# Performance work log

Measured on AMD Instinct MI355X. Metric: run time of the kernel, lower is better.

## Reference

```python
import jax, jax.numpy as jnp
import numpy as np

B, TK, H = 32, 1024, 512
N = 2 * H          # hidden_dim * 2
AD = 512           # attention_dimension


def setup_inputs() -> dict:
    key = jax.random.key(0)
    ks = jax.random.split(key, 11)
    s = 0.02  # weight scale
    return {
        's_t_hat': jax.random.normal(ks[0], (B, N), jnp.float32),
        'encoder_outputs': jax.random.normal(ks[1], (B, TK, N), jnp.float32),
        'encoder_feature': jax.random.normal(ks[2], (B * TK, N), jnp.float32),
        'enc_padding_mask': jax.random.uniform(ks[3], (B, TK), jnp.float32),
        'coverage': jax.random.uniform(ks[4], (B, TK), jnp.float32),
        'r_i': jax.random.normal(ks[5], (B, TK, AD), jnp.float32),
        'W_s_w': jax.random.normal(ks[6], (N, N), jnp.float32) * s,
        'W_s_b': jax.random.normal(ks[7], (N,), jnp.float32) * s,
        'W_c_w': jax.random.normal(ks[8], (N, 1), jnp.float32) * s,
        'v_w': jax.random.normal(ks[9], (1, N), jnp.float32) * s,
        'W_r_w': jax.random.normal(ks[10], (N, AD), jnp.float32) * s,
    }


def reference(s_t_hat, encoder_outputs, encoder_feature, enc_padding_mask,
              coverage, r_i, W_s_w, W_s_b, W_c_w, v_w, W_r_w):
    b, t_k, n = encoder_outputs.shape
    # decoder feature: W_s(s_t_hat), broadcast over time
    dec_fea = s_t_hat @ W_s_w.T + W_s_b                       # [b, n]
    enc_feat = encoder_feature.reshape(b, t_k, n)             # [b, t_k, n]
    # coverage feature: W_c applied to scalar coverage per position
    cov_feat = coverage[..., None] * W_c_w[:, 0]              # [b, t_k, n]
    e = jnp.tanh(enc_feat + dec_fea[:, None, :] + cov_feat)   # [b, t_k, n]
    scores = jnp.einsum('btn,n->bt', e, v_w[0])               # [b, t_k]
    attn_ = jax.nn.softmax(scores, axis=1) * enc_padding_mask
    attn = attn_ / attn_.sum(1, keepdims=True)                # renormalized
    c_t = jnp.einsum('bt,btn->bn', attn, encoder_outputs)     # [b, n]
    coverage_new = coverage + attn                            # [b, t_k]
    # structural (LSA) branch
    Wrri = jnp.einsum('bta,na->btn', r_i, W_r_w)              # [b, t_k, n]
    e_s = jnp.tanh(Wrri + dec_fea[:, None, :])
    s2 = jnp.einsum('btn,n->bt', e_s, v_w[0])
    a_struct = (jax.nn.softmax(s2, axis=1) * enc_padding_mask)[:, None, :]  # [b,1,t_k]
    c_t_struct = jnp.einsum('bt,btn->bn', a_struct[:, 0], encoder_outputs)  # [b, n]
    return (c_t, attn, coverage_new, c_t_struct, a_struct)
```

## Files before the change

### kernel.cpp

```cpp
#include <hip/hip_runtime.h>
#include <hip/hip_bf16.h>

static constexpr int BB   = 32;
static constexpr int TKK  = 1024;
static constexpr int ND   = 1024;
static constexpr int ADIM = 512;

typedef __attribute__((ext_vector_type(8))) short bf16x8;
typedef __attribute__((ext_vector_type(4))) float f32x4;

__device__ __forceinline__ float fast_tanh(float x) {
  x = fminf(fmaxf(x, -15.f), 15.f);
  float e = __expf(2.f * x);
  return __fdividef(e - 1.f, e + 1.f);
}

__device__ __forceinline__ short f2bf(float x) {
  unsigned u = __float_as_uint(x);
  u += 0x7FFF + ((u >> 16) & 1);
  return (short)(u >> 16);
}

__device__ __forceinline__ void gload_lds16(const void* g, void* l) {
  __builtin_amdgcn_global_load_lds(
      (const __attribute__((address_space(1))) unsigned int*)g,
      (__attribute__((address_space(3))) unsigned int*)l, 16, 0, 0);
}

__global__ __launch_bounds__(256) void k_cvt2(const float* __restrict__ r_i,
    const float* __restrict__ Wr, short* __restrict__ rb, short* __restrict__ wb) {
  size_t bid = blockIdx.x;
  const float* src;
  short* dst;
  size_t i;
  if (bid < 8192) { src = r_i; dst = rb; i = bid * 256 + threadIdx.x; }
  else            { src = Wr;  dst = wb; i = (bid - 8192) * 256 + threadIdx.x; }
  float4 a = ((const float4*)src)[2 * i];
  float4 b = ((const float4*)src)[2 * i + 1];
  bf16x8 h;
  h[0] = f2bf(a.x); h[1] = f2bf(a.y); h[2] = f2bf(a.z); h[3] = f2bf(a.w);
  h[4] = f2bf(b.x); h[5] = f2bf(b.y); h[6] = f2bf(b.z); h[7] = f2bf(b.w);
  ((bf16x8*)dst)[i] = h;
}

__global__ __launch_bounds__(256) void k_decfea(const float* __restrict__ s_t_hat,
    const float* __restrict__ Wsw, const float* __restrict__ Wsb,
    float* __restrict__ dec) {
  int b  = blockIdx.x >> 3;
  int n0 = (blockIdx.x & 7) << 7;
  int w = threadIdx.x >> 6, lane = threadIdx.x & 63;
  const float4* s4 = (const float4*)(s_t_hat + (size_t)b * ND);
  float4 sv0 = s4[lane], sv1 = s4[lane + 64], sv2 = s4[lane + 128], sv3 = s4[lane + 192];
  for (int nn = 0; nn < 32; nn++) {
    int n = n0 + w * 32 + nn;
    const float4* w4 = (const float4*)(Wsw + (size_t)n * ND);
    float4 wa = w4[lane], wb = w4[lane + 64], wc = w4[lane + 128], wd = w4[lane + 192];
    float acc = sv0.x*wa.x + sv0.y*wa.y + sv0.z*wa.z + sv0.w*wa.w
              + sv1.x*wb.x + sv1.y*wb.y + sv1.z*wb.z + sv1.w*wb.w
              + sv2.x*wc.x + sv2.y*wc.y + sv2.z*wc.z + sv2.w*wc.w
              + sv3.x*wd.x + sv3.y*wd.y + sv3.z*wd.z + sv3.w*wd.w;
    #pragma unroll
    for (int off = 32; off; off >>= 1) acc += __shfl_down(acc, off);
    if (lane == 0) dec[b * ND + n] = acc + Wsb[n];
  }
}

__global__ __launch_bounds__(256) void k_scoresA(const float* __restrict__ ef,
    const float* __restrict__ dec, const float* __restrict__ Wc,
    const float* __restrict__ vw, const float* __restrict__ cov,
    float* __restrict__ scores) {
  const int bt0 = blockIdx.x * 8 + (threadIdx.x >> 6) * 2;
  const int lane = threadIdx.x & 63;
  const int b0 = bt0 >> 10, b1 = (bt0 + 1) >> 10;
  const float c0 = cov[bt0], c1 = cov[bt0 + 1];
  float s0 = 0.f, s1 = 0.f;
  #pragma unroll
  for (int q = 0; q < 4; ++q) {
    const int col = q * 256 + lane * 4;
    float4 e0 = *(const float4*)(ef + (size_t)bt0 * ND + col);
    float4 e1 = *(const float4*)(ef + (size_t)(bt0 + 1) * ND + col);
    float4 d0 = *(const float4*)(dec + (size_t)b0 * ND + col);
    float4 d1 = *(const float4*)(dec + (size_t)b1 * ND + col);
    float4 w = *(const float4*)(Wc + col);
    float4 v = *(const float4*)(vw + col);
    s0 += v.x * fast_tanh(e0.x + d0.x + c0 * w.x)
        + v.y * fast_tanh(e0.y + d0.y + c0 * w.y)
        + v.z * fast_tanh(e0.z + d0.z + c0 * w.z)
        + v.w * fast_tanh(e0.w + d0.w + c0 * w.w);
    s1 += v.x * fast_tanh(e1.x + d1.x + c1 * w.x)
        + v.y * fast_tanh(e1.y + d1.y + c1 * w.y)
        + v.z * fast_tanh(e1.z + d1.z + c1 * w.z)
        + v.w * fast_tanh(e1.w + d1.w + c1 * w.w);
  }
  #pragma unroll
  for (int off = 32; off; off >>= 1) {
    s0 += __shfl_down(s0, off);
    s1 += __shfl_down(s1, off);
  }
  if (lane == 0) {
    scores[bt0]     = s0;
    scores[bt0 + 1] = s1;
  }
}

__global__ __launch_bounds__(256) void k_softmaxA(const float* __restrict__ scores,
    const float* __restrict__ mask, const float* __restrict__ cov,
    float* __restrict__ attn, float* __restrict__ covnew) {
  __shared__ float sb[4];
  int b = blockIdx.x, tid = threadIdx.x;
  float4 s = *(const float4*)(scores + (size_t)b * TKK + tid * 4);
  float m = fmaxf(fmaxf(s.x, s.y), fmaxf(s.z, s.w));
  #pragma unroll
  for (int off = 32; off; off >>= 1) m = fmaxf(m, __shfl_down(m, off));
  if ((tid & 63) == 0) sb[tid >> 6] = m;
  __syncthreads();
  m = fmaxf(fmaxf(sb[0], sb[1]), fmaxf(sb[2], sb[3]));
  float4 mk = *(const float4*)(mask + (size_t)b * TKK + tid * 4);
  float4 e;
  e.x = __expf(s.x - m) * mk.x;
  e.y = __expf(s.y - m) * mk.y;
  e.z = __expf(s.z - m) * mk.z;
  e.w = __expf(s.w - m) * mk.w;
  float sum = e.x + e.y + e.z + e.w;
  #pragma unroll
  for (int off = 32; off; off >>= 1) sum += __shfl_down(sum, off);
  __syncthreads();
  if ((tid & 63) == 0) sb[tid >> 6] = sum;
  __syncthreads();
  float inv = __fdividef(1.f, sb[0] + sb[1] + sb[2] + sb[3]);
  float4 a = {e.x * inv, e.y * inv, e.z * inv, e.w * inv};
  *(float4*)(attn + (size_t)b * TKK + tid * 4) = a;
  float4 c = *(const float4*)(cov + (size_t)b * TKK + tid * 4);
  float4 cn = {c.x + a.x, c.y + a.y, c.z + a.z, c.w + a.w};
  *(float4*)(covnew + (size_t)b * TKK + tid * 4) = cn;
}

__global__ __launch_bounds__(256) void k_gemmB3(const short* __restrict__ rb,
    const short* __restrict__ wb, const float* __restrict__ dec,
    const float* __restrict__ vw, float* __restrict__ part) {
  __shared__ __align__(16) short As[3][128 * 32];
  __shared__ __align__(16) short Bs[3][128 * 32];
  const int tid = threadIdx.x;
  const int lane = tid & 63, wv = tid >> 6;
  const int wm = wv >> 1, wn = wv & 1;
  const int g = lane >> 4, cl = lane & 15;
  const int bid = blockIdx.x;
  const int swz = (bid & 7) * 256 + (bid >> 3);
  const int mchunk = swz >> 3, nchunk = swz & 7;
  const int b  = mchunk >> 3;
  const int t0 = (mchunk & 7) * 128;
  const int n0 = nchunk * 128;
  const int lrow4 = lane >> 2;
  const int sck   = ((lane & 3) ^ ((lane >> 3) & 3)) * 8;
  const short* Agbase = rb + (size_t)(b * TKK + t0) * ADIM;
  const short* Bgbase = wb + (size_t)n0 * ADIM;
  const int rdsw = (g ^ ((cl >> 1) & 3)) * 8;

  f32x4 acc[4][4];
  #pragma unroll
  for (int m = 0; m < 4; ++m)
    #pragma unroll
    for (int n = 0; n < 4; ++n) acc[m][n] = (f32x4){0.f, 0.f, 0.f, 0.f};

  auto stage = [&](int buf, int kc) {
    const int k0 = kc * 32;
    #pragma unroll
    for (int p = 0; p < 2; ++p) {
      const int rowc = p * 64 + wv * 16;
      const int row  = rowc + lrow4;
      gload_lds16(Agbase + (size_t)row * ADIM + k0 + sck, &As[buf][rowc * 32]);
      gload_lds16(Bgbase + (size_t)row * ADIM + k0 + sck, &Bs[buf][rowc * 32]);
    }
  };

  stage(0, 0);
  stage(1, 1);
  for (int kc = 0; kc < 16; ++kc) {
    if (kc < 14) {
      stage((kc + 2) % 3, kc + 2);
      asm volatile("s_waitcnt vmcnt(8)" ::: "memory");
    } else if (kc == 14) {
      asm volatile("s_waitcnt vmcnt(4)" ::: "memory");
    } else {
      asm volatile("s_waitcnt vmcnt(0)" ::: "memory");
    }
    __builtin_amdgcn_s_barrier();
    const int cur = kc % 3;
    bf16x8 af[4], bfr[4];
    #pragma unroll
    for (int m = 0; m < 4; ++m)
      af[m] = *(const bf16x8*)&As[cur][(wm * 64 + m * 16 + cl) * 32 + rdsw];
    #pragma unroll
    for (int n = 0; n < 4; ++n)
      bfr[n] = *(const bf16x8*)&Bs[cur][(wn * 64 + n * 16 + cl) * 32 + rdsw];
    #pragma unroll
    for (int m = 0; m < 4; ++m)
      #pragma unroll
      for (int n = 0; n < 4; ++n)
        acc[m][n] = __builtin_amdgcn_mfma_f32_16x16x32_bf16(af[m], bfr[n], acc[m][n], 0, 0, 0);
    __builtin_amdgcn_s_barrier();
  }

  float vvv[4], ddd[4];
  #pragma unroll
  for (int n = 0; n < 4; ++n) {
    const int col = n0 + wn * 64 + n * 16 + cl;
    vvv[n] = vw[col];
    ddd[n] = dec[b * ND + col];
  }
  #pragma unroll
  for (int m = 0; m < 4; ++m) {
    #pragma unroll
    for (int r = 0; r < 4; ++r) {
      float s = 0.f;
      #pragma unroll
      for (int n = 0; n < 4; ++n)
        s += vvv[n] * fast_tanh(acc[m][n][r] + ddd[n]);
      #pragma unroll
      for (int off = 1; off < 16; off <<= 1) s += __shfl_xor(s, off);
      if (cl == 0) {
        const int rowg = b * TKK + t0 + wm * 64 + m * 16 + g * 4 + r;
        part[(size_t)rowg * 16 + nchunk * 2 + wn] = s;
      }
    }
  }
}

__global__ __launch_bounds__(256) void k_gemmB(const float* __restrict__ r_i,
    const float* __restrict__ Wr, const float* __restrict__ dec,
    const float* __restrict__ vw, float* __restrict__ part) {
  __shared__ short As[128 * 64];
  __shared__ short Bs[128 * 64];
  const int tid = threadIdx.x;
  const int lane = tid & 63, wv = tid >> 6;
  const int wm = wv >> 1, wn = wv & 1;
  const int g = lane >> 4, cl = lane & 15;
  const int mchunk = blockIdx.x, nchunk = blockIdx.y;
  const int b  = mchunk >> 3;
  const int t0 = (mchunk & 7) * 128;
  const int n0 = nchunk * 128;
  const float* Ag = r_i + (size_t)(b * TKK + t0) * ADIM;
  const float* Bg = Wr + (size_t)n0 * ADIM;
  const int srow = tid >> 3, skk = (tid & 7) * 8;

  f32x4 acc[4][4];
  #pragma unroll
  for (int m = 0; m < 4; ++m)
    #pragma unroll
    for (int n = 0; n < 4; ++n) acc[m][n] = (f32x4){0.f, 0.f, 0.f, 0.f};

  for (int kc = 0; kc < 8; ++kc) {
    const int k0 = kc * 64;
    __syncthreads();
    #pragma unroll
    for (int dit = 0; dit < 4; ++dit) {
      const int row = dit * 32 + srow;
      const float* sa = Ag + (size_t)row * ADIM + k0 + skk;
      float4 a0 = *(const float4*)sa, a1 = *(const float4*)(sa + 4);
      bf16x8 ha;
      ha[0]=f2bf(a0.x); ha[1]=f2bf(a0.y); ha[2]=f2bf(a0.z); ha[3]=f2bf(a0.w);
      ha[4]=f2bf(a1.x); ha[5]=f2bf(a1.y); ha[6]=f2bf(a1.z); ha[7]=f2bf(a1.w);
      *(bf16x8*)&As[row * 64 + skk] = ha;
      const float* sbp = Bg + (size_t)row * ADIM + k0 + skk;
      float4 b0 = *(const float4*)sbp, b1 = *(const float4*)(sbp + 4);
      bf16x8 hb;
      hb[0]=f2bf(b0.x); hb[1]=f2bf(b0.y); hb[2]=f2bf(b0.z); hb[3]=f2bf(b0.w);
      hb[4]=f2bf(b1.x); hb[5]=f2bf(b1.y); hb[6]=f2bf(b1.z); hb[7]=f2bf(b1.w);
      *(bf16x8*)&Bs[row * 64 + skk] = hb;
    }
    __syncthreads();
    #pragma unroll
    for (int kf = 0; kf < 2; ++kf) {
      bf16x8 af[4], bfr[4];
      #pragma unroll
      for (int m = 0; m < 4; ++m)
        af[m] = *(const bf16x8*)&As[(wm * 64 + m * 16 + cl) * 64 + kf * 32 + g * 8];
      #pragma unroll
      for (int n = 0; n < 4; ++n)
        bfr[n] = *(const bf16x8*)&Bs[(wn * 64 + n * 16 + cl) * 64 + kf * 32 + g * 8];
      #pragma unroll
      for (int m = 0; m < 4; ++m)
        #pragma unroll
        for (int n = 0; n < 4; ++n)
          acc[m][n] = __builtin_amdgcn_mfma_f32_16x16x32_bf16(af[m], bfr[n], acc[m][n], 0, 0, 0);
    }
  }
  float vvv[4], ddd[4];
  #pragma unroll
  for (int n = 0; n < 4; ++n) {
    const int col = n0 + wn * 64 + n * 16 + cl;
    vvv[n] = vw[col];
    ddd[n] = dec[b * ND + col];
  }
  #pragma unroll
  for (int m = 0; m < 4; ++m) {
    #pragma unroll
    for (int r = 0; r < 4; ++r) {
      float s = 0.f;
      #pragma unroll
      for (int n = 0; n < 4; ++n)
        s += vvv[n] * fast_tanh(acc[m][n][r] + ddd[n]);
      #pragma unroll
      for (int off = 1; off < 16; off <<= 1) s += __shfl_xor(s, off);
      if (cl == 0) {
        const int rowg = b * TKK + t0 + wm * 64 + m * 16 + g * 4 + r;
        part[(size_t)rowg * 16 + nchunk * 2 + wn] = s;
      }
    }
  }
}

__global__ __launch_bounds__(256) void k_softmaxB(const float* __restrict__ part,
    const float* __restrict__ mask, float* __restrict__ astruct) {
  __shared__ float sb[4];
  int b = blockIdx.x, tid = threadIdx.x;
  float sv[4];
  #pragma unroll
  for (int tt = 0; tt < 4; ++tt) {
    const float4* pp = (const float4*)(part + ((size_t)b * TKK + tid * 4 + tt) * 16);
    float4 q0 = pp[0], q1 = pp[1], q2 = pp[2], q3 = pp[3];
    sv[tt] = q0.x+q0.y+q0.z+q0.w + q1.x+q1.y+q1.z+q1.w
           + q2.x+q2.y+q2.z+q2.w + q3.x+q3.y+q3.z+q3.w;
  }
  float m = fmaxf(fmaxf(sv[0], sv[1]), fmaxf(sv[2], sv[3]));
  #pragma unroll
  for (int off = 32; off; off >>= 1) m = fmaxf(m, __shfl_down(m, off));
  if ((tid & 63) == 0) sb[tid >> 6] = m;
  __syncthreads();
  m = fmaxf(fmaxf(sb[0], sb[1]), fmaxf(sb[2], sb[3]));
  float e0 = __expf(sv[0] - m), e1 = __expf(sv[1] - m);
  float e2 = __expf(sv[2] - m), e3 = __expf(sv[3] - m);
  float sum = e0 + e1 + e2 + e3;
  #pragma unroll
  for (int off = 32; off; off >>= 1) sum += __shfl_down(sum, off);
  __syncthreads();
  if ((tid & 63) == 0) sb[tid >> 6] = sum;
  __syncthreads();
  float inv = __fdividef(1.f, sb[0] + sb[1] + sb[2] + sb[3]);
  float4 mk = *(const float4*)(mask + (size_t)b * TKK + tid * 4);
  float4 a = {e0 * mk.x * inv, e1 * mk.y * inv, e2 * mk.z * inv, e3 * mk.w * inv};
  *(float4*)(astruct + (size_t)b * TKK + tid * 4) = a;
}

__global__ __launch_bounds__(256) void k_ctx(const float* __restrict__ enc,
    const float* __restrict__ attn, const float* __restrict__ astr,
    float* __restrict__ partials) {
  int tc = blockIdx.x, b = blockIdx.y;
  int tid = threadIdx.x, lane = tid & 63;
  const float4* e4 = (const float4*)(enc + (size_t)(b * TKK + tc * 32) * ND);
  float a1v = attn[(size_t)b * TKK + tc * 32 + (lane & 31)];
  float a2v = astr[(size_t)b * TKK + tc * 32 + (lane & 31)];
  float4 ac = {0, 0, 0, 0}, as = {0, 0, 0, 0};
  #pragma unroll 8
  for (int m = 0; m < 32; m++) {
    float a1 = __shfl(a1v, m), a2 = __shfl(a2v, m);
    float4 ev = e4[(size_t)m * 256 + tid];
    ac.x += a1 * ev.x; ac.y += a1 * ev.y; ac.z += a1 * ev.z; ac.w += a1 * ev.w;
    as.x += a2 * ev.x; as.y += a2 * ev.y; as.z += a2 * ev.z; as.w += a2 * ev.w;
  }
  float* p = partials + (size_t)(b * 32 + tc) * 2 * ND;
  *(float4*)(p + tid * 4) = ac;
  *(float4*)(p + ND + tid * 4) = as;
}

__global__ __launch_bounds__(256) void k_reduce(const float* __restrict__ partials,
    float* __restrict__ ct, float* __restrict__ cts) {
  int b = blockIdx.x, cx = blockIdx.y;
  int col = cx * 256 + threadIdx.x;
  float sc = 0.f, ss = 0.f;
  for (int tc = 0; tc < 32; tc++) {
    const float* p = partials + (size_t)(b * 32 + tc) * 2 * ND;
    sc += p[col];
    ss += p[ND + col];
  }
  ct[(size_t)b * ND + col] = sc;
  cts[(size_t)b * ND + col] = ss;
}

extern "C" void kernel_launch(void* const* d_in, const int* in_sizes, int n_in,
                              void* d_out, int out_size, void* d_ws, size_t ws_size,
                              hipStream_t stream) {
  const float* s_t_hat = (const float*)d_in[0];
  const float* enc_out  = (const float*)d_in[1];
  const float* enc_feat = (const float*)d_in[2];
  const float* mask     = (const float*)d_in[3];
  const float* cov      = (const float*)d_in[4];
  const float* r_i      = (const float*)d_in[5];
  const float* Wsw      = (const float*)d_in[6];
  const float* Wsb      = (const float*)d_in[7];
  const float* Wc       = (const float*)d_in[8];
  const float* vw       = (const float*)d_in[9];
  const float* Wr       = (const float*)d_in[10];

  float* out    = (float*)d_out;
  float* ct     = out;
  float* attn   = out + 32768;
  float* covnew = out + 65536;
  float* cts    = out + 98304;
  float* astr   = out + 131072;

  float* ws       = (float*)d_ws;
  float* dec      = ws;
  float* scores   = ws + 32768;
  float* s2part   = ws + 65536;
  float* partials = ws + 589824;
  short* rb       = (short*)(ws + 2686976);
  short* wb       = rb + 16777216;
  const size_t NEEDED = 2686976ull * 4 + 16777216ull * 2 + 524288ull * 2;

  k_decfea<<<256, 256, 0, stream>>>(s_t_hat, Wsw, Wsb, dec);
  k_scoresA<<<4096, 256, 0, stream>>>(enc_feat, dec, Wc, vw, cov, scores);
  k_softmaxA<<<BB, 256, 0, stream>>>(scores, mask, cov, attn, covnew);
  if (ws_size >= NEEDED) {
    k_cvt2<<<8448, 256, 0, stream>>>(r_i, Wr, rb, wb);
    k_gemmB3<<<2048, 256, 0, stream>>>(rb, wb, dec, vw, s2part);
  } else {
    k_gemmB<<<dim3(256, 8), 256, 0, stream>>>(r_i, Wr, dec, vw, s2part);
  }
  k_softmaxB<<<BB, 256, 0, stream>>>(s2part, mask, astr);
  k_ctx<<<dim3(32, BB), 256, 0, stream>>>(enc_out, attn, astr, partials);
  k_reduce<<<dim3(BB, 4), 256, 0, stream>>>(partials, ct, cts);
}
```

Before: 171.8 us.

## Merge branch-A scoring into GEMM launch and fuse both softmaxes

Adds the branch-A score computation to the bf16 MFMA GEMM kernel as an extra 4096 blocks, so the memory-bound tanh scoring and the compute-bound GEMM run concurrently in one launch. The two per-batch softmax kernels are combined into a single 64-block launch, removing two kernel launches and their serialization gaps. The cost is a larger grid whose blocks all reserve the GEMM's LDS allocation, which may lower occupancy for the scoring blocks. The fallback path's scoresA is rewritten to one row per wave.

```diff
diff --git a/kernel.cpp b/kernel.cpp
--- a/kernel.cpp
+++ b/kernel.cpp
@@ -69,159 +69,153 @@
     const float* __restrict__ dec, const float* __restrict__ Wc,
     const float* __restrict__ vw, const float* __restrict__ cov,
     float* __restrict__ scores) {
-  const int bt0 = blockIdx.x * 8 + (threadIdx.x >> 6) * 2;
+  const int bt = blockIdx.x * 4 + (threadIdx.x >> 6);
+  const int b  = bt >> 10;
   const int lane = threadIdx.x & 63;
-  const int b0 = bt0 >> 10, b1 = (bt0 + 1) >> 10;
-  const float c0 = cov[bt0], c1 = cov[bt0 + 1];
-  float s0 = 0.f, s1 = 0.f;
+  const float c = cov[bt];
+  float s = 0.f;
   #pragma unroll
   for (int q = 0; q < 4; ++q) {
     const int col = q * 256 + lane * 4;
-    float4 e0 = *(const float4*)(ef + (size_t)bt0 * ND + col);
-    float4 e1 = *(const float4*)(ef + (size_t)(bt0 + 1) * ND + col);
-    float4 d0 = *(const float4*)(dec + (size_t)b0 * ND + col);
-    float4 d1 = *(const float4*)(dec + (size_t)b1 * ND + col);
+    float4 e = *(const float4*)(ef + (size_t)bt * ND + col);
+    float4 d = *(const float4*)(dec + (size_t)b * ND + col);
     float4 w = *(const float4*)(Wc + col);
     float4 v = *(const float4*)(vw + col);
-    s0 += v.x * fast_tanh(e0.x + d0.x + c0 * w.x)
-        + v.y * fast_tanh(e0.y + d0.y + c0 * w.y)
-        + v.z * fast_tanh(e0.z + d0.z + c0 * w.z)
-        + v.w * fast_tanh(e0.w + d0.w + c0 * w.w);
-    s1 += v.x * fast_tanh(e1.x + d1.x + c1 * w.x)
-        + v.y * fast_tanh(e1.y + d1.y + c1 * w.y)
-        + v.z * fast_tanh(e1.z + d1.z + c1 * w.z)
-        + v.w * fast_tanh(e1.w + d1.w + c1 * w.w);
+    s += v.x * fast_tanh(e.x + d.x + c * w.x)
+       + v.y * fast_tanh(e.y + d.y + c * w.y)
+       + v.z * fast_tanh(e.z + d.z + c * w.z)
+       + v.w * fast_tanh(e.w + d.w + c * w.w);
   }
   #pragma unroll
-  for (int off = 32; off; off >>= 1) {
-    s0 += __shfl_down(s0, off);
-    s1 += __shfl_down(s1, off);
-  }
-  if (lane == 0) {
-    scores[bt0]     = s0;
-    scores[bt0 + 1] = s1;
-  }
-}
-
-__global__ __launch_bounds__(256) void k_softmaxA(const float* __restrict__ scores,
-    const float* __restrict__ mask, const float* __restrict__ cov,
-    float* __restrict__ attn, float* __restrict__ covnew) {
-  __shared__ float sb[4];
-  int b = blockIdx.x, tid = threadIdx.x;
-  float4 s = *(const float4*)(scores + (size_t)b * TKK + tid * 4);
-  float m = fmaxf(fmaxf(s.x, s.y), fmaxf(s.z, s.w));
-  #pragma unroll
-  for (int off = 32; off; off >>= 1) m = fmaxf(m, __shfl_down(m, off));
-  if ((tid & 63) == 0) sb[tid >> 6] = m;
-  __syncthreads();
-  m = fmaxf(fmaxf(sb[0], sb[1]), fmaxf(sb[2], sb[3]));
-  float4 mk = *(const float4*)(mask + (size_t)b * TKK + tid * 4);
-  float4 e;
-  e.x = __expf(s.x - m) * mk.x;
-  e.y = __expf(s.y - m) * mk.y;
-  e.z = __expf(s.z - m) * mk.z;
-  e.w = __expf(s.w - m) * mk.w;
-  float sum = e.x + e.y + e.z + e.w;
-  #pragma unroll
-  for (int off = 32; off; off >>= 1) sum += __shfl_down(sum, off);
-  __syncthreads();
-  if ((tid & 63) == 0) sb[tid >> 6] = sum;
-  __syncthreads();
-  float inv = __fdividef(1.f, sb[0] + sb[1] + sb[2] + sb[3]);
-  float4 a = {e.x * inv, e.y * inv, e.z * inv, e.w * inv};
-  *(float4*)(attn + (size_t)b * TKK + tid * 4) = a;
-  float4 c = *(const float4*)(cov + (size_t)b * TKK + tid * 4);
-  float4 cn = {c.x + a.x, c.y + a.y, c.z + a.z, c.w + a.w};
-  *(float4*)(covnew + (size_t)b * TKK + tid * 4) = cn;
-}
-
-__global__ __launch_bounds__(256) void k_gemmB3(const short* __restrict__ rb,
+  for (int off = 32; off; off >>= 1) s += __shfl_down(s, off);
+  if (lane == 0) scores[bt] = s;
+}
+
+__global__ __launch_bounds__(256) void k_mega(const short* __restrict__ rb,
     const short* __restrict__ wb, const float* __restrict__ dec,
-    const float* __restrict__ vw, float* __restrict__ part) {
-  __shared__ __align__(16) short As[3][128 * 32];
-  __shared__ __align__(16) short Bs[3][128 * 32];
-  const int tid = threadIdx.x;
-  const int lane = tid & 63, wv = tid >> 6;
-  const int wm = wv >> 1, wn = wv & 1;
-  const int g = lane >> 4, cl = lane & 15;
-  const int bid = blockIdx.x;
-  const int swz = (bid & 7) * 256 + (bid >> 3);
-  const int mchunk = swz >> 3, nchunk = swz & 7;
-  const int b  = mchunk >> 3;
-  const int t0 = (mchunk & 7) * 128;
-  const int n0 = nchunk * 128;
-  const int lrow4 = lane >> 2;
-  const int sck   = ((lane & 3) ^ ((lane >> 3) & 3)) * 8;
-  const short* Agbase = rb + (size_t)(b * TKK + t0) * ADIM;
-  const short* Bgbase = wb + (size_t)n0 * ADIM;
-  const int rdsw = (g ^ ((cl >> 1) & 3)) * 8;
-
-  f32x4 acc[4][4];
-  #pragma unroll
-  for (int m = 0; m < 4; ++m)
-    #pragma unroll
-    for (int n = 0; n < 4; ++n) acc[m][n] = (f32x4){0.f, 0.f, 0.f, 0.f};
-
-  auto stage = [&](int buf, int kc) {
-    const int k0 = kc * 32;
-    #pragma unroll
-    for (int p = 0; p < 2; ++p) {
-      const int rowc = p * 64 + wv * 16;
-      const int row  = rowc + lrow4;
-      gload_lds16(Agbase + (size_t)row * ADIM + k0 + sck, &As[buf][rowc * 32]);
-      gload_lds16(Bgbase + (size_t)row * ADIM + k0 + sck, &Bs[buf][rowc * 32]);
-    }
-  };
-
-  stage(0, 0);
-  stage(1, 1);
-  for (int kc = 0; kc < 16; ++kc) {
-    if (kc < 14) {
-      stage((kc + 2) % 3, kc + 2);
-      asm volatile("s_waitcnt vmcnt(8)" ::: "memory");
-    } else if (kc == 14) {
-      asm volatile("s_waitcnt vmcnt(4)" ::: "memory");
-    } else {
-      asm volatile("s_waitcnt vmcnt(0)" ::: "memory");
-    }
-    __builtin_amdgcn_s_barrier();
-    const int cur = kc % 3;
-    bf16x8 af[4], bfr[4];
+    const float* __restrict__ vw, float* __restrict__ part,
+    const float* __restrict__ ef, const float* __restrict__ Wc,
+    const float* __restrict__ cov, float* __restrict__ scores) {
+  if (blockIdx.x < 2048) {
+    __shared__ __align__(16) short As[3][128 * 32];
+    __shared__ __align__(16) short Bs[3][128 * 32];
+    const int tid = threadIdx.x;
+    const int lane = tid & 63, wv = tid >> 6;
+    const int wm = wv >> 1, wn = wv & 1;
+    const int g = lane >> 4, cl = lane & 15;
+    const int bid = blockIdx.x;
+    const int swz = (bid & 7) * 256 + (bid >> 3);
+    const int mchunk = swz >> 3, nchunk = swz & 7;
+    const int b  = mchunk >> 3;
+    const int t0 = (mchunk & 7) * 128;
+    const int n0 = nchunk * 128;
+    const int lrow4 = lane >> 2;
+    const int sck   = ((lane & 3) ^ ((lane >> 3) & 3)) * 8;
+    const short* Agbase = rb + (size_t)(b * TKK + t0) * ADIM;
+    const short* Bgbase = wb + (size_t)n0 * ADIM;
+    const int rdsw = (g ^ ((cl >> 1) & 3)) * 8;
+
+    f32x4 acc[4][4];
     #pragma unroll
     for (int m = 0; m < 4; ++m)
-      af[m] = *(const bf16x8*)&As[cur][(wm * 64 + m * 16 + cl) * 32 + rdsw];
-    #pragma unroll
-    for (int n = 0; n < 4; ++n)
-      bfr[n] = *(const bf16x8*)&Bs[cur][(wn * 64 + n * 16 + cl) * 32 + rdsw];
-    #pragma unroll
-    for (int m = 0; m < 4; ++m)
+      #pragma unroll
+      for (int n = 0; n < 4; ++n) acc[m][n] = (f32x4){0.f, 0.f, 0.f, 0.f};
+
+    auto stage = [&](int buf, int kc) {
+      const int k0 = kc * 32;
+      #pragma unroll
+      for (int p = 0; p < 2; ++p) {
+        const int rowc = p * 64 + wv * 16;
+        const int row  = rowc + lrow4;
+        gload_lds16(Agbase + (size_t)row * ADIM + k0 + sck, &As[buf][rowc * 32]);
+        gload_lds16(Bgbase + (size_t)row * ADIM + k0 + sck, &Bs[buf][rowc * 32]);
+      }
+    };
+
+    stage(0, 0);
+    stage(1, 1);
+    for (int kc = 0; kc < 16; ++kc) {
+      if (kc < 14) {
+        stage((kc + 2) % 3, kc + 2);
+        asm volatile("s_waitcnt vmcnt(8)" ::: "memory");
+      } else if (kc == 14) {
+        asm volatile("s_waitcnt vmcnt(4)" ::: "memory");
+      } else {
+        asm volatile("s_waitcnt vmcnt(0)" ::: "memory");
+      }
+      __builtin_amdgcn_s_barrier();
+      const int cur = kc % 3;
+      bf16x8 af[4], bfr[4];
+      #pragma unroll
+      for (int m = 0; m < 4; ++m)
+        af[m] = *(const bf16x8*)&As[cur][(wm * 64 + m * 16 + cl) * 32 + rdsw];
       #pragma unroll
       for (int n = 0; n < 4; ++n)
-        acc[m][n] = __builtin_amdgcn_mfma_f32_16x16x32_bf16(af[m], bfr[n], acc[m][n], 0, 0, 0);
-    __builtin_amdgcn_s_barrier();
-  }
-
-  float vvv[4], ddd[4];
-  #pragma unroll
-  for (int n = 0; n < 4; ++n) {
-    const int col = n0 + wn * 64 + n * 16 + cl;
-    vvv[n] = vw[col];
-    ddd[n] = dec[b * ND + col];
-  }
-  #pragma unroll
-  for (int m = 0; m < 4; ++m) {
-    #pragma unroll
-    for (int r = 0; r < 4; ++r) {
-      float s = 0.f;
-      #pragma unroll
-      for (int n = 0; n < 4; ++n)
-        s += vvv[n] * fast_tanh(acc[m][n][r] + ddd[n]);
-      #pragma unroll
-      for (int off = 1; off < 16; off <<= 1) s += __shfl_xor(s, off);
-      if (cl == 0) {
-        const int rowg = b * TKK + t0 + wm * 64 + m * 16 + g * 4 + r;
-        part[(size_t)rowg * 16 + nchunk * 2 + wn] = s;
+        bfr[n] = *(const bf16x8*)&Bs[cur][(wn * 64 + n * 16 + cl) * 32 + rdsw];
+      #pragma unroll
+      for (int m = 0; m < 4; ++m)
+        #pragma unroll
+        for (int n = 0; n < 4; ++n)
+          acc[m][n] = __builtin_amdgcn_mfma_f32_16x16x32_bf16(af[m], bfr[n], acc[m][n], 0, 0, 0);
+      __builtin_amdgcn_s_barrier();
+    }
+
+    float vvv[4], ddd[4];
+    #pragma unroll
+    for (int n = 0; n < 4; ++n) {
+      const int col = n0 + wn * 64 + n * 16 + cl;
+      vvv[n] = vw[col];
+      ddd[n] = dec[b * ND + col];
+    }
+    #pragma unroll
+    for (int m = 0; m < 4; ++m) {
+      #pragma unroll
+      for (int r = 0; r < 4; ++r) {
+        float s = 0.f;
+        #pragma unroll
+        for (int n = 0; n < 4; ++n)
+          s += vvv[n] * fast_tanh(acc[m][n][r] + ddd[n]);
+        #pragma unroll
+        for (int off = 1; off < 16; off <<= 1) s += __shfl_xor(s, off);
+        if (cl == 0) {
+          const int rowg = b * TKK + t0 + wm * 64 + m * 16 + g * 4 + r;
+          part[(size_t)rowg * 16 + nchunk * 2 + wn] = s;
+        }
       }
+    }
+  } else {
+    const int sbid = blockIdx.x - 2048;
+    const int bt0 = sbid * 8 + (threadIdx.x >> 6) * 2;
+    const int lane = threadIdx.x & 63;
+    const int b0 = bt0 >> 10, b1 = (bt0 + 1) >> 10;
+    const float c0 = cov[bt0], c1 = cov[bt0 + 1];
+    float s0 = 0.f, s1 = 0.f;
+    #pragma unroll
+    for (int q = 0; q < 4; ++q) {
+      const int col = q * 256 + lane * 4;
+      float4 e0 = *(const float4*)(ef + (size_t)bt0 * ND + col);
+      float4 e1 = *(const float4*)(ef + (size_t)(bt0 + 1) * ND + col);
+      float4 d0 = *(const float4*)(dec + (size_t)b0 * ND + col);
+      float4 d1 = *(const float4*)(dec + (size_t)b1 * ND + col);
+      float4 w = *(const float4*)(Wc + col);
+      float4 v = *(const float4*)(vw + col);
+      s0 += v.x * fast_tanh(e0.x + d0.x + c0 * w.x)
+          + v.y * fast_tanh(e0.y + d0.y + c0 * w.y)
+          + v.z * fast_tanh(e0.z + d0.z + c0 * w.z)
+          + v.w * fast_tanh(e0.w + d0.w + c0 * w.w);
+      s1 += v.x * fast_tanh(e1.x + d1.x + c1 * w.x)
+          + v.y * fast_tanh(e1.y + d1.y + c1 * w.y)
+          + v.z * fast_tanh(e1.z + d1.z + c1 * w.z)
+          + v.w * fast_tanh(e1.w + d1.w + c1 * w.w);
+    }
+    #pragma unroll
+    for (int off = 32; off; off >>= 1) {
+      s0 += __shfl_down(s0, off);
+      s1 += __shfl_down(s1, off);
+    }
+    if (lane == 0) {
+      scores[bt0]     = s0;
+      scores[bt0 + 1] = s1;
     }
   }
 }
@@ -310,36 +304,68 @@
   }
 }
 
-__global__ __launch_bounds__(256) void k_softmaxB(const float* __restrict__ part,
-    const float* __restrict__ mask, float* __restrict__ astruct) {
+__global__ __launch_bounds__(256) void k_softmaxAB(const float* __restrict__ scores,
+    const float* __restrict__ part, const float* __restrict__ mask,
+    const float* __restrict__ cov, float* __restrict__ attn,
+    float* __restrict__ covnew, float* __restrict__ astruct) {
   __shared__ float sb[4];
-  int b = blockIdx.x, tid = threadIdx.x;
-  float sv[4];
-  #pragma unroll
-  for (int tt = 0; tt < 4; ++tt) {
-    const float4* pp = (const float4*)(part + ((size_t)b * TKK + tid * 4 + tt) * 16);
-    float4 q0 = pp[0], q1 = pp[1], q2 = pp[2], q3 = pp[3];
-    sv[tt] = q0.x+q0.y+q0.z+q0.w + q1.x+q1.y+q1.z+q1.w
-           + q2.x+q2.y+q2.z+q2.w + q3.x+q3.y+q3.z+q3.w;
-  }
-  float m = fmaxf(fmaxf(sv[0], sv[1]), fmaxf(sv[2], sv[3]));
-  #pragma unroll
-  for (int off = 32; off; off >>= 1) m = fmaxf(m, __shfl_down(m, off));
-  if ((tid & 63) == 0) sb[tid >> 6] = m;
-  __syncthreads();
-  m = fmaxf(fmaxf(sb[0], sb[1]), fmaxf(sb[2], sb[3]));
-  float e0 = __expf(sv[0] - m), e1 = __expf(sv[1] - m);
-  float e2 = __expf(sv[2] - m), e3 = __expf(sv[3] - m);
-  float sum = e0 + e1 + e2 + e3;
-  #pragma unroll
-  for (int off = 32; off; off >>= 1) sum += __shfl_down(sum, off);
-  __syncthreads();
-  if ((tid & 63) == 0) sb[tid >> 6] = sum;
-  __syncthreads();
-  float inv = __fdividef(1.f, sb[0] + sb[1] + sb[2] + sb[3]);
-  float4 mk = *(const float4*)(mask + (size_t)b * TKK + tid * 4);
-  float4 a = {e0 * mk.x * inv, e1 * mk.y * inv, e2 * mk.z * inv, e3 * mk.w * inv};
-  *(float4*)(astruct + (size_t)b * TKK + tid * 4) = a;
+  int tid = threadIdx.x;
+  if (blockIdx.x < 32) {
+    int b = blockIdx.x;
+    float4 s = *(const float4*)(scores + (size_t)b * TKK + tid * 4);
+    float m = fmaxf(fmaxf(s.x, s.y), fmaxf(s.z, s.w));
+    #pragma unroll
+    for (int off = 32; off; off >>= 1) m = fmaxf(m, __shfl_down(m, off));
+    if ((tid & 63) == 0) sb[tid >> 6] = m;
+    __syncthreads();
+    m = fmaxf(fmaxf(sb[0], sb[1]), fmaxf(sb[2], sb[3]));
+    float4 mk = *(const float4*)(mask + (size_t)b * TKK + tid * 4);
+    float4 e;
+    e.x = __expf(s.x - m) * mk.x;
+    e.y = __expf(s.y - m) * mk.y;
+    e.z = __expf(s.z - m) * mk.z;
+    e.w = __expf(s.w - m) * mk.w;
+    float sum = e.x + e.y + e.z + e.w;
+    #pragma unroll
+    for (int off = 32; off; off >>= 1) sum += __shfl_down(sum, off);
+    __syncthreads();
+    if ((tid & 63) == 0) sb[tid >> 6] = sum;
+    __syncthreads();
+    float inv = __fdividef(1.f, sb[0] + sb[1] + sb[2] + sb[3]);
+    float4 a = {e.x * inv, e.y * inv, e.z * inv, e.w * inv};
+    *(float4*)(attn + (size_t)b * TKK + tid * 4) = a;
+    float4 c = *(const float4*)(cov + (size_t)b * TKK + tid * 4);
+    float4 cn = {c.x + a.x, c.y + a.y, c.z + a.z, c.w + a.w};
+    *(float4*)(covnew + (size_t)b * TKK + tid * 4) = cn;
+  } else {
+    int b = blockIdx.x - 32;
+    float sv[4];
+    #pragma unroll
+    for (int tt = 0; tt < 4; ++tt) {
+      const float4* pp = (const float4*)(part + ((size_t)b * TKK + tid * 4 + tt) * 16);
+      float4 q0 = pp[0], q1 = pp[1], q2 = pp[2], q3 = pp[3];
+      sv[tt] = q0.x+q0.y+q0.z+q0.w + q1.x+q1.y+q1.z+q1.w
+             + q2.x+q2.y+q2.z+q2.w + q3.x+q3.y+q3.z+q3.w;
+    }
+    float m = fmaxf(fmaxf(sv[0], sv[1]), fmaxf(sv[2], sv[3]));
+    #pragma unroll
+    for (int off = 32; off; off >>= 1) m = fmaxf(m, __shfl_down(m, off));
+    if ((tid & 63) == 0) sb[tid >> 6] = m;
+    __syncthreads();
+    m = fmaxf(fmaxf(sb[0], sb[1]), fmaxf(sb[2], sb[3]));
+    float e0 = __expf(sv[0] - m), e1 = __expf(sv[1] - m);
+    float e2 = __expf(sv[2] - m), e3 = __expf(sv[3] - m);
+    float sum = e0 + e1 + e2 + e3;
+    #pragma unroll
+    for (int off = 32; off; off >>= 1) sum += __shfl_down(sum, off);
+    __syncthreads();
+    if ((tid & 63) == 0) sb[tid >> 6] = sum;
+    __syncthreads();
+    float inv = __fdividef(1.f, sb[0] + sb[1] + sb[2] + sb[3]);
+    float4 mk = *(const float4*)(mask + (size_t)b * TKK + tid * 4);
+    float4 a = {e0 * mk.x * inv, e1 * mk.y * inv, e2 * mk.z * inv, e3 * mk.w * inv};
+    *(float4*)(astruct + (size_t)b * TKK + tid * 4) = a;
+  }
 }
 
 __global__ __launch_bounds__(256) void k_ctx(const float* __restrict__ enc,
@@ -409,15 +435,15 @@
   const size_t NEEDED = 2686976ull * 4 + 16777216ull * 2 + 524288ull * 2;
 
   k_decfea<<<256, 256, 0, stream>>>(s_t_hat, Wsw, Wsb, dec);
-  k_scoresA<<<4096, 256, 0, stream>>>(enc_feat, dec, Wc, vw, cov, scores);
-  k_softmaxA<<<BB, 256, 0, stream>>>(scores, mask, cov, attn, covnew);
   if (ws_size >= NEEDED) {
     k_cvt2<<<8448, 256, 0, stream>>>(r_i, Wr, rb, wb);
-    k_gemmB3<<<2048, 256, 0, stream>>>(rb, wb, dec, vw, s2part);
+    k_mega<<<6144, 256, 0, stream>>>(rb, wb, dec, vw, s2part,
+                                     enc_feat, Wc, cov, scores);
   } else {
+    k_scoresA<<<8192, 256, 0, stream>>>(enc_feat, dec, Wc, vw, cov, scores);
     k_gemmB<<<dim3(256, 8), 256, 0, stream>>>(r_i, Wr, dec, vw, s2part);
   }
-  k_softmaxB<<<BB, 256, 0, stream>>>(s2part, mask, astr);
+  k_softmaxAB<<<64, 256, 0, stream>>>(scores, s2part, mask, cov, attn, covnew, astr);
   k_ctx<<<dim3(32, BB), 256, 0, stream>>>(enc_out, attn, astr, partials);
   k_reduce<<<dim3(BB, 4), 256, 0, stream>>>(partials, ct, cts);
 }
```

Result: faster. 163.1 us (median of 3 runs) (-5.1%).
